# Performance work log

Hardware: AMD Instinct MI355X
Metric: run time of the kernel (lower is better)

## Reference

```python
import jax, jax.numpy as jnp
import numpy as np

B, T, E, H = 4, 2048, 512, 8
D = E // H  # head_dim = 64


def setup_inputs() -> dict:
    key = jax.random.key(0)
    ks = jax.random.split(key, 9)
    s = 1.0 / np.sqrt(E)
    inp = {
        "x": jax.random.normal(ks[0], (B, T, E), dtype=jnp.float32),
        "Wq": jax.random.normal(ks[1], (E, E), dtype=jnp.float32) * s,
        "bq": jnp.zeros((E,), dtype=jnp.float32),
        "Wk": jax.random.normal(ks[2], (E, E), dtype=jnp.float32) * s,
        "bk": jnp.zeros((E,), dtype=jnp.float32),
        "Wv": jax.random.normal(ks[3], (E, E), dtype=jnp.float32) * s,
        "bv": jnp.zeros((E,), dtype=jnp.float32),
        "Wo": jax.random.normal(ks[4], (E, E), dtype=jnp.float32) * s,
        "bo": jnp.zeros((E,), dtype=jnp.float32),
    }
    return inp


def reference(x, Wq, bq, Wk, bk, Wv, bv, Wo, bo):
    # x: (B, T, E); weights stored (in, out) so y = x @ W + b
    b, t, _ = x.shape
    q = (x @ Wq + bq).reshape(b, t, H, D).transpose(0, 2, 1, 3)  # (B,H,T,D)
    k = (x @ Wk + bk).reshape(b, t, H, D).transpose(0, 2, 1, 3)  # (B,H,T,D)
    v = (x @ Wv + bv).reshape(b, t, H, D).transpose(0, 2, 1, 3)  # (B,H,T,D)
    scores = jnp.einsum("bhqd,bhkd->bhqk", q, k) / np.sqrt(D)    # (B,H,Tq,Tk)
    # faithful to source: softmax over dim=-2 (the query axis)
    attn = jax.nn.softmax(scores, axis=-2)
    out = jnp.einsum("bhqk,bhkd->bhqd", attn, v)                  # (B,H,T,D)
    # faithful to source: reshape (B,H,T,D) -> (B,T,H*D) with NO transpose
    out = out.reshape(b, t, H * D)
    return out @ Wo + bo
```

## Files before the change

### kernel.cpp

```cpp
#include <hip/hip_runtime.h>
#include <hip/hip_bf16.h>

#define NB 4
#define NT 2048
#define NE 512
#define NH 8
#define ND 64
#define BH (NB*NH)

typedef __attribute__((ext_vector_type(8))) short short8;
typedef __attribute__((ext_vector_type(4))) short short4v;
typedef __attribute__((ext_vector_type(4))) float f32x4;

typedef const __attribute__((address_space(3))) short* lds_sp;

__device__ __forceinline__ f32x4 mfma16(short8 a, short8 b, f32x4 c){
  return __builtin_amdgcn_mfma_f32_16x16x32_bf16(a, b, c, 0, 0, 0);
}
__device__ __forceinline__ short f2b(float f){
  union { float f; unsigned u; } v; v.f = f;
  unsigned r = v.u + 0x7FFFu + ((v.u >> 16) & 1u);
  return (short)(r >> 16);
}
__device__ __forceinline__ float b2f(short s){
  union { unsigned u; float f; } v; v.u = ((unsigned)(unsigned short)s) << 16; return v.f;
}
__device__ __forceinline__ unsigned pk2(float a, float b){
  union { __hip_bfloat162 h; unsigned u; } v;
  v.h = __float22bfloat162_rn(make_float2(a, b));
  return v.u;
}
__device__ __forceinline__ void gld16(const void* g, void* l){
  __builtin_amdgcn_global_load_lds((const __attribute__((address_space(1))) void*)g,
                                   (__attribute__((address_space(3))) void*)l, 16, 0, 0);
}
__device__ __forceinline__ short4v trr(lds_sp p, int imm){
  short4v r;
  asm volatile("ds_read_b64_tr_b16 %0, %1 offset:%2" : "=v"(r) : "v"(p), "i"(imm));
  return r;
}

__global__ __launch_bounds__(256) void pack_x_k(const float* __restrict__ x, short* __restrict__ xb){
  int i = blockIdx.x*256 + threadIdx.x;
  f32x4 a = ((const f32x4*)x)[2*i];
  f32x4 b = ((const f32x4*)x)[2*i+1];
  union { short8 s; unsigned u[4]; } o;
  o.u[0] = pk2(a[0], a[1]);
  o.u[1] = pk2(a[2], a[3]);
  o.u[2] = pk2(b[0], b[1]);
  o.u[3] = pk2(b[2], b[3]);
  ((short8*)xb)[i] = o.s;
}

__global__ __launch_bounds__(256) void pack_wt_k(const float* __restrict__ Wq, const float* __restrict__ Wk,
                                                 const float* __restrict__ Wv, const float* __restrict__ Wo,
                                                 short* __restrict__ Wt){
  const float* W = blockIdx.z==0?Wq: blockIdx.z==1?Wk: blockIdx.z==2?Wv:Wo;
  short* out = Wt + (size_t)blockIdx.z*NE*NE;
  __shared__ float t[32][33];
  int tx = threadIdx.x & 31, ty = threadIdx.x >> 5;
  int j0 = blockIdx.x*32, e0 = blockIdx.y*32;
#pragma unroll
  for (int r = 0; r < 4; ++r)
    t[ty*4+r][tx] = W[(size_t)(e0+ty*4+r)*NE + j0+tx];
  __syncthreads();
#pragma unroll
  for (int r = 0; r < 4; ++r)
    out[(size_t)(j0+ty*4+r)*NE + e0+tx] = f2b(t[tx][ty*4+r]);
}

__global__ __launch_bounds__(256) void gemm_qkv_k(const short* __restrict__ xb, const short* __restrict__ Wt,
                                                  const float* __restrict__ bq, const float* __restrict__ bk,
                                                  const float* __restrict__ bv,
                                                  short* __restrict__ Q, short* __restrict__ K, short* __restrict__ V){
  int z = blockIdx.z;
  const short* Bm = Wt + (size_t)z*NE*NE;
  const float* bias = z==0?bq: z==1?bk:bv;
  short* out = z==0?Q: z==1?K:V;
  float scale = (z==0) ? 0.125f : 1.0f;

  __shared__ short As[128*32];
  __shared__ short Bs[128*32];
  int tid = threadIdx.x, lane = tid & 63, wid = tid >> 6;
  int m0 = blockIdx.y*128, n0 = blockIdx.x*128;
  int wm = wid >> 1, wn = wid & 1;
  int sr = lane >> 2, sg = lane & 3;
  int fr = lane & 15, fg = lane >> 4;

  f32x4 acc[4][4] = {};

  for (int kt = 0; kt < 16; ++kt){
    int k0 = kt*32;
    {
      int ii0 = wid*2, ii1 = wid*2+1;
      int r0 = ii0*16 + sr, r1 = ii1*16 + sr;
      gld16(xb + (size_t)(m0 + r0)*NE + k0 + ((sg ^ (r0&3))<<3), (short*)As + ii0*512);
      gld16(xb + (size_t)(m0 + r1)*NE + k0 + ((sg ^ (r1&3))<<3), (short*)As + ii1*512);
      gld16(Bm + (size_t)(n0 + r0)*NE + k0 + ((sg ^ (r0&3))<<3), (short*)Bs + ii0*512);
      gld16(Bm + (size_t)(n0 + r1)*NE + k0 + ((sg ^ (r1&3))<<3), (short*)Bs + ii1*512);
    }
    __syncthreads();
    short8 af[4], bf[4];
#pragma unroll
    for (int m = 0; m < 4; ++m){
      int row = wm*64 + m*16 + fr;
      af[m] = *(const short8*)&As[row*32 + ((fg ^ (row&3))<<3)];
    }
#pragma unroll
    for (int n = 0; n < 4; ++n){
      int row = wn*64 + n*16 + fr;
      bf[n] = *(const short8*)&Bs[row*32 + ((fg ^ (row&3))<<3)];
    }
#pragma unroll
    for (int m = 0; m < 4; ++m)
#pragma unroll
      for (int n = 0; n < 4; ++n)
        acc[m][n] = mfma16(af[m], bf[n], acc[m][n]);
    __syncthreads();
  }
#pragma unroll
  for (int m = 0; m < 4; ++m)
#pragma unroll
    for (int n = 0; n < 4; ++n)
#pragma unroll
      for (int i = 0; i < 4; ++i){
        int row = m0 + wm*64 + m*16 + fg*4 + i;
        int col = n0 + wn*64 + n*16 + fr;
        float v = (acc[m][n][i] + bias[col]) * scale;
        int b = row >> 11, t = row & (NT-1), h = col >> 6, d = col & 63;
        out[(((size_t)(b*NH + h)*NT + t)<<6) + d] = f2b(v);
      }
}

__global__ __launch_bounds__(512, 4) void attn_l_k(const short* __restrict__ Q, const short* __restrict__ K,
                                                   const short* __restrict__ V, short* __restrict__ Vp){
  int bid = blockIdx.x;
  int bh = (bid & 7)*4 + ((bid >> 3) & 3);
  int kt = bid >> 5;
  const short* Qh = Q + (size_t)bh*NT*ND;
  const short* Kh = K + (size_t)bh*NT*ND;
  __shared__ short Qs0[8192];
  __shared__ short Qs1[8192];
  __shared__ float rl_all[128];
  int tid = threadIdx.x, lane = tid&63, wid = tid>>6;
  int fr = lane&15, fg = lane>>4;
  int sr = lane>>3, sg = lane&7;

  int krow = kt*128 + wid*16;
  short8 ak[2];
#pragma unroll
  for (int dh = 0; dh < 2; ++dh)
    ak[dh] = *(const short8*)&Kh[(size_t)(krow + fr)*ND + dh*32 + fg*8];

  const short* qsrc0 = Qh + (size_t)(wid*16 + sr)*ND + ((sg ^ sr)<<3);
  const short* qsrc1 = qsrc0 + 8*ND;
  auto stageQ = [&](short* qb, int t){
    size_t adv = (size_t)t*128*ND;
    gld16(qsrc0 + adv, qb + wid*1024);
    gld16(qsrc1 + adv, qb + wid*1024 + 512);
  };

  float rs[4] = {0.f,0.f,0.f,0.f};

  auto computeQ = [&](const short* Qt){
#pragma unroll
    for (int qf = 0; qf < 8; ++qf){
      int row = qf*16 + fr;
      short8 b0 = *(const short8*)&Qt[row*64 + ((fg ^ (row&7))<<3)];
      short8 b1 = *(const short8*)&Qt[row*64 + (((4+fg) ^ (row&7))<<3)];
      f32x4 c = {};
      c = mfma16(ak[0], b0, c);
      c = mfma16(ak[1], b1, c);
#pragma unroll
      for (int i = 0; i < 4; ++i)
        rs[i] += __expf(c[i]);
    }
  };

  stageQ(Qs0, 0);
  __syncthreads();

  for (int qt2 = 0; qt2 < 8; ++qt2){
    int qtA = qt2*2;
    stageQ(Qs1, qtA+1);
    computeQ(Qs0);
    __syncthreads();
    if (qtA+2 < 16) stageQ(Qs0, qtA+2);
    computeQ(Qs1);
    __syncthreads();
  }

#pragma unroll
  for (int i = 0; i < 4; ++i){
    float v = rs[i];
    v += __shfl_xor(v, 1); v += __shfl_xor(v, 2);
    v += __shfl_xor(v, 4); v += __shfl_xor(v, 8);
    if (fr == 0) rl_all[wid*16 + fg*4 + i] = 1.0f / v;
  }
  {
    int row = tid >> 2;
    int col0 = (tid & 3) * 16;
    float inv = rl_all[row];
    const short* vsrc = V  + (size_t)bh*NT*ND + (size_t)(kt*128 + row)*ND + col0;
    short*       vdst = Vp + (size_t)bh*NT*ND + (size_t)(kt*128 + row)*ND + col0;
    short8 v0 = *(const short8*)vsrc;
    short8 v1 = *(const short8*)(vsrc + 8);
    union { short8 s; unsigned u[4]; } o0, o1;
#pragma unroll
    for (int j = 0; j < 4; ++j){
      o0.u[j] = pk2(b2f(v0[2*j])*inv, b2f(v0[2*j+1])*inv);
      o1.u[j] = pk2(b2f(v1[2*j])*inv, b2f(v1[2*j+1])*inv);
    }
    *(short8*)vdst       = o0.s;
    *(short8*)(vdst + 8) = o1.s;
  }
}

__global__ __launch_bounds__(256, 3) void attn_out_k(const short* __restrict__ Q, const short* __restrict__ K,
                                                     const short* __restrict__ Vp,
                                                     short* __restrict__ out2){
  int bid = blockIdx.x;
  int xcd = bid & 7, w = bid >> 3;
  int bh = xcd*4 + (w & 3);
  int q0 = (w >> 2) * 128;
  int b = bh >> 3, h = bh & 7;
  const short* Qh = Q + (size_t)bh*NT*ND;
  const short* Kh = K + (size_t)bh*NT*ND;
  const short* Vh = Vp + (size_t)bh*NT*ND;
  __shared__ short S0[8192];
  __shared__ short S1[8192];
  int tid = threadIdx.x, lane = tid&63, wid = tid>>6;
  int fr = lane&15, fg = lane>>4;
  int sr = lane>>3, sg = lane&7;
  int qw = q0 + wid*32;

  short8 qreg[2][2];
#pragma unroll
  for (int qf = 0; qf < 2; ++qf)
#pragma unroll
    for (int dh = 0; dh < 2; ++dh)
      qreg[qf][dh] = *(const short8*)&Qh[(size_t)(qw + qf*16 + fr)*ND + dh*32 + fg*8];

  const short* ksrc0 = Kh + (size_t)(wid*16 + sr)*ND + ((sg ^ sr)<<3);
  const short* ksrc1 = ksrc0 + 8*ND;
  int vt0 = wid*4 + (lane>>5);
  int vt1 = vt0 + 2;
  int vr = (lane&31)>>1, vc0 = (lane&1)*8;
  const short* vsrc0 = Vh + (size_t)((vt0>>2)*16 + vr)*ND + (vt0&3)*16 + vc0;
  const short* vsrc1 = Vh + (size_t)((vt1>>2)*16 + vr)*ND + (vt1&3)*16 + vc0;

  auto stage2 = [&](short* sb, int t){
    size_t adv = (size_t)t*64*ND;
    gld16(ksrc0 + adv, sb + wid*1024);
    gld16(ksrc1 + adv, sb + wid*1024 + 512);
    gld16(vsrc0 + adv, sb + 4096 + wid*1024);
    gld16(vsrc1 + adv, sb + 4096 + wid*1024 + 512);
  };

  f32x4 oacc[2][4] = {};

  auto compute = [&](const short* Ks, const short* Vs){
    short8 ak[4][2];
#pragma unroll
    for (int rf = 0; rf < 4; ++rf){
      int row = rf*16 + fr;
#pragma unroll
      for (int dh = 0; dh < 2; ++dh)
        ak[rf][dh] = *(const short8*)&Ks[row*64 + (((dh*4+fg) ^ (row&7))<<3)];
    }
    short8 pa[2][2];
#pragma unroll
    for (int qf = 0; qf < 2; ++qf){
      f32x4 s[4];
      __builtin_amdgcn_s_setprio(1);
#pragma unroll
      for (int rf = 0; rf < 4; ++rf){
        f32x4 c = {};
        c = mfma16(ak[rf][0], qreg[qf][0], c);
        c = mfma16(ak[rf][1], qreg[qf][1], c);
        s[rf] = c;
      }
      __builtin_amdgcn_s_setprio(0);
#pragma unroll
      for (int c = 0; c < 2; ++c){
        union { short8 s8; unsigned u[4]; } p;
        p.u[0] = pk2(__expf(s[2*c  ][0]), __expf(s[2*c  ][1]));
        p.u[1] = pk2(__expf(s[2*c  ][2]), __expf(s[2*c  ][3]));
        p.u[2] = pk2(__expf(s[2*c+1][0]), __expf(s[2*c+1][1]));
        p.u[3] = pk2(__expf(s[2*c+1][2]), __expf(s[2*c+1][3]));
        pa[qf][c] = p.s8;
      }
    }

    lds_sp vbase = (lds_sp)(Vs + lane*4);
#pragma unroll
    for (int c = 0; c < 2; ++c){
      short4v t0[4], t1[4];
#pragma unroll
      for (int n = 0; n < 4; ++n){
        t0[n] = trr(vbase, ((2*c  )*4 + n)*512);
        t1[n] = trr(vbase, ((2*c+1)*4 + n)*512);
      }
      asm volatile("s_waitcnt lgkmcnt(0)");
      __builtin_amdgcn_sched_barrier(0);
      __builtin_amdgcn_s_setprio(1);
#pragma unroll
      for (int n = 0; n < 4; ++n){
        short8 vb = __builtin_shufflevector(t0[n], t1[n], 0,1,2,3,4,5,6,7);
#pragma unroll
        for (int qf = 0; qf < 2; ++qf)
          oacc[qf][n] = mfma16(pa[qf][c], vb, oacc[qf][n]);
      }
      __builtin_amdgcn_s_setprio(0);
    }
  };

  stage2(S0, 0);
  __syncthreads();

  for (int kt2 = 0; kt2 < 16; ++kt2){
    int ktA = kt2*2;
    stage2(S1, ktA+1);
    compute(S0, S0 + 4096);
    __syncthreads();
    if (ktA+2 < 32) stage2(S0, ktA+2);
    compute(S1, S1 + 4096);
    __syncthreads();
  }

#pragma unroll
  for (int qf = 0; qf < 2; ++qf)
#pragma unroll
    for (int n = 0; n < 4; ++n)
#pragma unroll
      for (int i = 0; i < 4; ++i){
        int t = qw + qf*16 + fg*4 + i;
        int d = n*16 + fr;
        int r = h*256 + (t>>3);
        int e = ((t&7)<<6) + d;
        out2[((size_t)(b*NT + r)<<9) + e] = f2b(oacc[qf][n][i]);
      }
}

__global__ __launch_bounds__(256) void gemm_out_k(const short* __restrict__ A, const short* __restrict__ Bm,
                                                  const float* __restrict__ bo, float* __restrict__ out){
  __shared__ short As[128*32];
  __shared__ short Bs[128*32];
  int tid = threadIdx.x, lane = tid & 63, wid = tid >> 6;
  int m0 = blockIdx.y*128, n0 = blockIdx.x*128;
  int wm = wid >> 1, wn = wid & 1;
  int sr = lane >> 2, sg = lane & 3;
  int fr = lane & 15, fg = lane >> 4;

  f32x4 acc[4][4] = {};

  for (int kt = 0; kt < 16; ++kt){
    int k0 = kt*32;
    {
      int ii0 = wid*2, ii1 = wid*2+1;
      int r0 = ii0*16 + sr, r1 = ii1*16 + sr;
      gld16(A  + (size_t)(m0 + r0)*NE + k0 + ((sg ^ (r0&3))<<3), (short*)As + ii0*512);
      gld16(A  + (size_t)(m0 + r1)*NE + k0 + ((sg ^ (r1&3))<<3), (short*)As + ii1*512);
      gld16(Bm + (size_t)(n0 + r0)*NE + k0 + ((sg ^ (r0&3))<<3), (short*)Bs + ii0*512);
      gld16(Bm + (size_t)(n0 + r1)*NE + k0 + ((sg ^ (r1&3))<<3), (short*)Bs + ii1*512);
    }
    __syncthreads();
    short8 af[4], bf[4];
#pragma unroll
    for (int m = 0; m < 4; ++m){
      int row = wm*64 + m*16 + fr;
      af[m] = *(const short8*)&As[row*32 + ((fg ^ (row&3))<<3)];
    }
#pragma unroll
    for (int n = 0; n < 4; ++n){
      int row = wn*64 + n*16 + fr;
      bf[n] = *(const short8*)&Bs[row*32 + ((fg ^ (row&3))<<3)];
    }
#pragma unroll
    for (int m = 0; m < 4; ++m)
#pragma unroll
      for (int n = 0; n < 4; ++n)
        acc[m][n] = mfma16(af[m], bf[n], acc[m][n]);
    __syncthreads();
  }
#pragma unroll
  for (int m = 0; m < 4; ++m)
#pragma unroll
    for (int n = 0; n < 4; ++n)
#pragma unroll
      for (int i = 0; i < 4; ++i){
        int row = m0 + wm*64 + m*16 + fg*4 + i;
        int col = n0 + wn*64 + n*16 + fr;
        out[(size_t)row*NE + col] = acc[m][n][i] + bo[col];
      }
}

extern "C" void kernel_launch(void* const* d_in, const int* in_sizes, int n_in,
                              void* d_out, int out_size, void* d_ws, size_t ws_size,
                              hipStream_t stream){
  const float* x  = (const float*)d_in[0];
  const float* Wq = (const float*)d_in[1];
  const float* bq = (const float*)d_in[2];
  const float* Wk = (const float*)d_in[3];
  const float* bk = (const float*)d_in[4];
  const float* Wv = (const float*)d_in[5];
  const float* bv = (const float*)d_in[6];
  const float* Wo = (const float*)d_in[7];
  const float* bo = (const float*)d_in[8];
  float* out = (float*)d_out;

  char* ws = (char*)d_ws;
  size_t off = 0;
  auto alloc = [&](size_t bytes){ void* p = ws + off; off = (off + bytes + 255) & ~(size_t)255; return p; };
  short* xb    = (short*)alloc((size_t)NB*NT*NE*2);
  short* Wt    = (short*)alloc((size_t)4*NE*NE*2);
  short* Qb    = (short*)alloc((size_t)NB*NT*NE*2);
  short* Kb    = (short*)alloc((size_t)NB*NT*NE*2);
  short* Vb    = (short*)alloc((size_t)NB*NT*NE*2);
  short* Vp    = (short*)alloc((size_t)NB*NT*NE*2);
  short* out2  = (short*)alloc((size_t)NB*NT*NE*2);
  (void)ws_size; (void)in_sizes; (void)n_in; (void)out_size;

  pack_x_k<<<dim3((NB*NT*NE/8)/256), dim3(256), 0, stream>>>(x, xb);
  pack_wt_k<<<dim3(NE/32, NE/32, 4), dim3(256), 0, stream>>>(Wq, Wk, Wv, Wo, Wt);
  gemm_qkv_k<<<dim3(NE/128, (NB*NT)/128, 3), dim3(256), 0, stream>>>(xb, Wt, bq, bk, bv, Qb, Kb, Vb);
  attn_l_k<<<dim3((NT/128)*BH), dim3(512), 0, stream>>>(Qb, Kb, Vb, Vp);
  attn_out_k<<<dim3((NT/128)*BH), dim3(256), 0, stream>>>(Qb, Kb, Vp, out2);
  gemm_out_k<<<dim3(NE/128, (NB*NT)/128), dim3(256), 0, stream>>>(out2, Wt + (size_t)3*NE*NE, bo, out);
}
```

Baseline: 115.0 us.

## Double-buffer LDS in QKV and output GEMMs; fold log2e into Q scale for exp2

Both GEMM kernels now keep two LDS buffers and stage the next K-tile while running MFMAs on the current one, cutting the barrier count per tile in half and overlapping global loads with compute. Separately, the Q projection scale now includes log2(e), so attention uses the hardware exp2 instruction directly instead of __expf, which multiplies before exponentiating. Doubling the shared memory per GEMM block may lower occupancy.

```diff
diff --git a/kernel.cpp b/kernel.cpp
--- a/kernel.cpp
+++ b/kernel.cpp
@@ -8,6 +8,8 @@
 #define ND 64
 #define BH (NB*NH)
 
+#define LOG2E 1.44269504088896340736f
+
 typedef __attribute__((ext_vector_type(8))) short short8;
 typedef __attribute__((ext_vector_type(4))) short short4v;
 typedef __attribute__((ext_vector_type(4))) float f32x4;
@@ -29,6 +31,13 @@
   union { __hip_bfloat162 h; unsigned u; } v;
   v.h = __float22bfloat162_rn(make_float2(a, b));
   return v.u;
+}
+__device__ __forceinline__ float fexp2(float x){
+#if __has_builtin(__builtin_amdgcn_exp2f)
+  return __builtin_amdgcn_exp2f(x);
+#else
+  return __expf(0.69314718055994530942f * x);
+#endif
 }
 __device__ __forceinline__ void gld16(const void* g, void* l){
   __builtin_amdgcn_global_load_lds((const __attribute__((address_space(1))) void*)g,
@@ -77,10 +86,10 @@
   const short* Bm = Wt + (size_t)z*NE*NE;
   const float* bias = z==0?bq: z==1?bk:bv;
   short* out = z==0?Q: z==1?K:V;
-  float scale = (z==0) ? 0.125f : 1.0f;
-
-  __shared__ short As[128*32];
-  __shared__ short Bs[128*32];
+  float scale = (z==0) ? 0.125f*LOG2E : 1.0f;
+
+  __shared__ short A0[128*32], B0[128*32];
+  __shared__ short A1[128*32], B1[128*32];
   int tid = threadIdx.x, lane = tid & 63, wid = tid >> 6;
   int m0 = blockIdx.y*128, n0 = blockIdx.x*128;
   int wm = wid >> 1, wn = wid & 1;
@@ -89,17 +98,16 @@
 
   f32x4 acc[4][4] = {};
 
-  for (int kt = 0; kt < 16; ++kt){
+  auto stageG = [&](short* Ad, short* Bd, int kt){
     int k0 = kt*32;
-    {
-      int ii0 = wid*2, ii1 = wid*2+1;
-      int r0 = ii0*16 + sr, r1 = ii1*16 + sr;
-      gld16(xb + (size_t)(m0 + r0)*NE + k0 + ((sg ^ (r0&3))<<3), (short*)As + ii0*512);
-      gld16(xb + (size_t)(m0 + r1)*NE + k0 + ((sg ^ (r1&3))<<3), (short*)As + ii1*512);
-      gld16(Bm + (size_t)(n0 + r0)*NE + k0 + ((sg ^ (r0&3))<<3), (short*)Bs + ii0*512);
-      gld16(Bm + (size_t)(n0 + r1)*NE + k0 + ((sg ^ (r1&3))<<3), (short*)Bs + ii1*512);
-    }
-    __syncthreads();
+    int ii0 = wid*2, ii1 = wid*2+1;
+    int r0 = ii0*16 + sr, r1 = ii1*16 + sr;
+    gld16(xb + (size_t)(m0 + r0)*NE + k0 + ((sg ^ (r0&3))<<3), Ad + ii0*512);
+    gld16(xb + (size_t)(m0 + r1)*NE + k0 + ((sg ^ (r1&3))<<3), Ad + ii1*512);
+    gld16(Bm + (size_t)(n0 + r0)*NE + k0 + ((sg ^ (r0&3))<<3), Bd + ii0*512);
+    gld16(Bm + (size_t)(n0 + r1)*NE + k0 + ((sg ^ (r1&3))<<3), Bd + ii1*512);
+  };
+  auto computeG = [&](const short* As, const short* Bs){
     short8 af[4], bf[4];
 #pragma unroll
     for (int m = 0; m < 4; ++m){
@@ -116,8 +124,21 @@
 #pragma unroll
       for (int n = 0; n < 4; ++n)
         acc[m][n] = mfma16(af[m], bf[n], acc[m][n]);
-    __syncthreads();
-  }
+  };
+
+  stageG(A0, B0, 0);
+  __syncthreads();
+
+  for (int kt2 = 0; kt2 < 8; ++kt2){
+    int ktA = kt2*2;
+    stageG(A1, B1, ktA+1);
+    computeG(A0, B0);
+    __syncthreads();
+    if (ktA+2 < 16) stageG(A0, B0, ktA+2);
+    computeG(A1, B1);
+    __syncthreads();
+  }
+
 #pragma unroll
   for (int m = 0; m < 4; ++m)
 #pragma unroll
@@ -173,7 +194,7 @@
       c = mfma16(ak[1], b1, c);
 #pragma unroll
       for (int i = 0; i < 4; ++i)
-        rs[i] += __expf(c[i]);
+        rs[i] += fexp2(c[i]);
     }
   };
 
@@ -284,10 +305,10 @@
 #pragma unroll
       for (int c = 0; c < 2; ++c){
         union { short8 s8; unsigned u[4]; } p;
-        p.u[0] = pk2(__expf(s[2*c  ][0]), __expf(s[2*c  ][1]));
-        p.u[1] = pk2(__expf(s[2*c  ][2]), __expf(s[2*c  ][3]));
-        p.u[2] = pk2(__expf(s[2*c+1][0]), __expf(s[2*c+1][1]));
-        p.u[3] = pk2(__expf(s[2*c+1][2]), __expf(s[2*c+1][3]));
+        p.u[0] = pk2(fexp2(s[2*c  ][0]), fexp2(s[2*c  ][1]));
+        p.u[1] = pk2(fexp2(s[2*c  ][2]), fexp2(s[2*c  ][3]));
+        p.u[2] = pk2(fexp2(s[2*c+1][0]), fexp2(s[2*c+1][1]));
+        p.u[3] = pk2(fexp2(s[2*c+1][2]), fexp2(s[2*c+1][3]));
         pa[qf][c] = p.s8;
       }
     }
@@ -344,8 +365,8 @@
 
 __global__ __launch_bounds__(256) void gemm_out_k(const short* __restrict__ A, const short* __restrict__ Bm,
                                                   const float* __restrict__ bo, float* __restrict__ out){
-  __shared__ short As[128*32];
-  __shared__ short Bs[128*32];
+  __shared__ short A0[128*32], B0[128*32];
+  __shared__ short A1[128*32], B1[128*32];
   int tid = threadIdx.x, lane = tid & 63, wid = tid >> 6;
   int m0 = blockIdx.y*128, n0 = blockIdx.x*128;
   int wm = wid >> 1, wn = wid & 1;
@@ -354,17 +375,16 @@
 
   f32x4 acc[4][4] = {};
 
-  for (int kt = 0; kt < 16; ++kt){
+  auto stageG = [&](short* Ad, short* Bd, int kt){
     int k0 = kt*32;
-    {
-      int ii0 = wid*2, ii1 = wid*2+1;
-      int r0 = ii0*16 + sr, r1 = ii1*16 + sr;
-      gld16(A  + (size_t)(m0 + r0)*NE + k0 + ((sg ^ (r0&3))<<3), (short*)As + ii0*512);
-      gld16(A  + (size_t)(m0 + r1)*NE + k0 + ((sg ^ (r1&3))<<3), (short*)As + ii1*512);
-      gld16(Bm + (size_t)(n0 + r0)*NE + k0 + ((sg ^ (r0&3))<<3), (short*)Bs + ii0*512);
-      gld16(Bm + (size_t)(n0 + r1)*NE + k0 + ((sg ^ (r1&3))<<3), (short*)Bs + ii1*512);
-    }
-    __syncthreads();
+    int ii0 = wid*2, ii1 = wid*2+1;
+    int r0 = ii0*16 + sr, r1 = ii1*16 + sr;
+    gld16(A  + (size_t)(m0 + r0)*NE + k0 + ((sg ^ (r0&3))<<3), Ad + ii0*512);
+    gld16(A  + (size_t)(m0 + r1)*NE + k0 + ((sg ^ (r1&3))<<3), Ad + ii1*512);
+    gld16(Bm + (size_t)(n0 + r0)*NE + k0 + ((sg ^ (r0&3))<<3), Bd + ii0*512);
+    gld16(Bm + (size_t)(n0 + r1)*NE + k0 + ((sg ^ (r1&3))<<3), Bd + ii1*512);
+  };
+  auto computeG = [&](const short* As, const short* Bs){
     short8 af[4], bf[4];
 #pragma unroll
     for (int m = 0; m < 4; ++m){
@@ -381,8 +401,21 @@
 #pragma unroll
       for (int n = 0; n < 4; ++n)
         acc[m][n] = mfma16(af[m], bf[n], acc[m][n]);
-    __syncthreads();
-  }
+  };
+
+  stageG(A0, B0, 0);
+  __syncthreads();
+
+  for (int kt2 = 0; kt2 < 8; ++kt2){
+    int ktA = kt2*2;
+    stageG(A1, B1, ktA+1);
+    computeG(A0, B0);
+    __syncthreads();
+    if (ktA+2 < 16) stageG(A0, B0, ktA+2);
+    computeG(A1, B1);
+    __syncthreads();
+  }
+
 #pragma unroll
   for (int m = 0; m < 4; ++m)
 #pragma unroll
```

After: 117.3 us. No clear change (+2.0%).
